# Optimization experiments

Measured on AMD Instinct MI355X. Metric: run time of the kernel, lower is better.

## Reference

```python
import jax, jax.numpy as jnp
import numpy as np
import math

C_S = 256
NUM_HEADS = 8
HEAD_DIM = 32
TOTAL = NUM_HEADS * HEAD_DIM
B, S, I = 1, 256, 256  # batch, msa sequences (column attn axis), residues
LN_EPS = 1e-5


def setup_inputs() -> dict:
    key = jax.random.key(0)
    ks = jax.random.split(key, 10)
    sc = 1.0 / math.sqrt(C_S)
    return {
        "msa": jax.random.normal(ks[0], (B, S, I, C_S), dtype=jnp.float32),
        "ln_gamma": jnp.ones((C_S,), dtype=jnp.float32),
        "ln_beta": jnp.zeros((C_S,), dtype=jnp.float32),
        "Wq": jax.random.normal(ks[1], (C_S, TOTAL), dtype=jnp.float32) * sc,
        "Wk": jax.random.normal(ks[2], (C_S, TOTAL), dtype=jnp.float32) * sc,
        "Wv": jax.random.normal(ks[3], (C_S, TOTAL), dtype=jnp.float32) * sc,
        "Wg": jax.random.normal(ks[4], (C_S, TOTAL), dtype=jnp.float32) * sc,
        "bg": jnp.zeros((TOTAL,), dtype=jnp.float32),
        "Wo": jax.random.normal(ks[5], (TOTAL, C_S), dtype=jnp.float32) * (1.0 / math.sqrt(TOTAL)),
        "bo": jnp.zeros((C_S,), dtype=jnp.float32),
    }


def reference(msa, ln_gamma, ln_beta, Wq, Wk, Wv, Wg, bg, Wo, bo):
    # LayerNorm over channel dim
    mu = jnp.mean(msa, axis=-1, keepdims=True)
    var = jnp.mean(jnp.square(msa - mu), axis=-1, keepdims=True)
    x = (msa - mu) * jax.lax.rsqrt(var + LN_EPS) * ln_gamma + ln_beta

    b, s, i, _ = x.shape
    hd = (NUM_HEADS, HEAD_DIM)
    Q = (x @ Wq).reshape(b, s, i, *hd)
    K = (x @ Wk).reshape(b, s, i, *hd)
    V = (x @ Wv).reshape(b, s, i, *hd)
    G = jax.nn.sigmoid((x @ Wg + bg).reshape(b, s, i, *hd))

    # column attention: contract over head_dim, attend over sequence axis s/t
    scores = jnp.einsum('bsihd,btihd->bihst', Q, K) / math.sqrt(HEAD_DIM)
    attn = jax.nn.softmax(scores, axis=-1)
    vals = jnp.einsum('bihst,btihd->bsihd', attn, V)

    vals = (G * vals).reshape(b, s, i, TOTAL)
    return vals @ Wo + bo
```

## Files before the change

kernel.cpp:

```cpp
#include <hip/hip_runtime.h>
#include <hip/hip_fp16.h>
#include <math.h>

#define C_S 256
#define NUM_HEADS 8
#define HEAD_DIM 32
#define TOTAL 256
#define S_DIM 256
#define I_DIM 256
#define NROWS (S_DIM * I_DIM)
#define LN_EPS 1e-5f
#define QSCALE 0.25503534f

typedef _Float16 f16x8 __attribute__((ext_vector_type(8)));
typedef __attribute__((ext_vector_type(4))) float f32x4;

__device__ __forceinline__ ushort f2h(float x) {
  return __half_as_ushort(__float2half(x));
}
__device__ __forceinline__ float h2f(ushort u) {
  return __half2float(__ushort_as_half(u));
}
__device__ __forceinline__ void gl16(const void* g, void* l) {
  __builtin_amdgcn_global_load_lds(
      (const __attribute__((address_space(1))) unsigned*)g,
      (__attribute__((address_space(3))) unsigned*)l, 16, 0, 0);
}

__global__ __launch_bounds__(256) void prep_w_kernel(
    const float* __restrict__ Wq, const float* __restrict__ Wk,
    const float* __restrict__ Wv, const float* __restrict__ Wg,
    const float* __restrict__ Wo,
    ushort* __restrict__ Wch, ushort* __restrict__ Woh) {
  const int b = blockIdx.x;
  const int mat = b >> 8, n = b & 255;
  const int k = threadIdx.x;
  const float* W = (mat == 0) ? Wq : (mat == 1) ? Wk
                  : (mat == 2) ? Wv : (mat == 3) ? Wg : Wo;
  ushort h = f2h(W[(size_t)k * 256 + n]);
  if (mat < 4) Wch[((size_t)(mat * 256 + n)) * 256 + k] = h;
  else         Woh[(size_t)n * 256 + k] = h;
}

__global__ __launch_bounds__(256) void prep_x_kernel(
    const float* __restrict__ msa, const float* __restrict__ gamma,
    const float* __restrict__ beta, ushort* __restrict__ Xh) {
  const int row  = blockIdx.x * 4 + (threadIdx.x >> 6);
  const int lane = threadIdx.x & 63;
  float4 v = ((const float4*)(msa + (size_t)row * C_S))[lane];
  float sum = v.x + v.y + v.z + v.w;
  float sq  = v.x*v.x + v.y*v.y + v.z*v.z + v.w*v.w;
  #pragma unroll
  for (int off = 1; off < 64; off <<= 1) {
    sum += __shfl_xor(sum, off);
    sq  += __shfl_xor(sq, off);
  }
  float mu = sum * (1.0f / 256.0f);
  float rs = rsqrtf(sq * (1.0f / 256.0f) - mu * mu + LN_EPS);
  float4 gv = ((const float4*)gamma)[lane];
  float4 bv = ((const float4*)beta)[lane];
  ushort4 hh;
  hh.x = f2h((v.x - mu) * rs * gv.x + bv.x);
  hh.y = f2h((v.y - mu) * rs * gv.y + bv.y);
  hh.z = f2h((v.z - mu) * rs * gv.z + bv.z);
  hh.w = f2h((v.w - mu) * rs * gv.w + bv.w);
  *(ushort4*)(Xh + (size_t)row * 256 + lane * 4) = hh;
}

__global__ __launch_bounds__(256, 3) void fused_attn_kernel(
    const ushort* __restrict__ Xh,
    const ushort* __restrict__ Wch,
    const float* __restrict__ bg,
    ushort* __restrict__ Oh) {
  __shared__ __align__(16) ushort Kls[256][40];
  __shared__ __align__(16) ushort Vth[32][264];
  __shared__ __align__(16) ushort Pls[256][32];

  const int bid = blockIdx.x;
  const int xcd = bid & 7, j = bid >> 3;
  const int h = j & 7;
  const int i = (xcd << 5) + (j >> 3);
  const int ih = i * NUM_HEADS + h;
  const int tid = threadIdx.x;
  const int wave = tid >> 6, lane = tid & 63;
  const int lr = lane & 15, quad = lane >> 4;
  const int s_base = wave * 64;
  const size_t hbase = (size_t)ih * (S_DIM * HEAD_DIM);

  const int lrb0 = lr & 1, lrb1 = (lr >> 1) & 1;
  const int qw  = quad ^ (lrb0 << 1);
  const int prd = (quad ^ (lr & 3)) << 3;

  const ushort* xr0 = Xh + ((size_t)(s_base + lr) * 256 + i) * 256 + quad * 8;
  const ushort* wr0 = Wch + ((size_t)(h * 32 + lr)) * 256 + quad * 8;

  f32x4 kacc[2][4] = {}, vacc[2][4] = {};
  #pragma unroll
  for (int kb = 0; kb < 8; ++kb) {
    f16x8 xb[4];
    #pragma unroll
    for (int nt = 0; nt < 4; ++nt)
      xb[nt] = *(const f16x8*)(xr0 + (size_t)nt * 16 * 65536 + kb * 32);
    f16x8 wk[2], wv[2];
    #pragma unroll
    for (int mt = 0; mt < 2; ++mt) {
      wk[mt] = *(const f16x8*)(wr0 + (size_t)1 * 65536 + mt * 4096 + kb * 32);
      wv[mt] = *(const f16x8*)(wr0 + (size_t)2 * 65536 + mt * 4096 + kb * 32);
    }
    #pragma unroll
    for (int mt = 0; mt < 2; ++mt)
      #pragma unroll
      for (int nt = 0; nt < 4; ++nt) {
        kacc[mt][nt] = __builtin_amdgcn_mfma_f32_16x16x32_f16(wk[mt], xb[nt], kacc[mt][nt], 0, 0, 0);
        vacc[mt][nt] = __builtin_amdgcn_mfma_f32_16x16x32_f16(xb[nt], wv[mt], vacc[mt][nt], 0, 0, 0);
      }
  }
  #pragma unroll
  for (int mt = 0; mt < 2; ++mt)
    #pragma unroll
    for (int nt = 0; nt < 4; ++nt) {
      const int t = s_base + nt * 16 + lr;
      ushort4 kp;
      kp.x = f2h(kacc[mt][nt][0]); kp.y = f2h(kacc[mt][nt][1]);
      kp.z = f2h(kacc[mt][nt][2]); kp.w = f2h(kacc[mt][nt][3]);
      *(ushort4*)&Kls[t][mt * 16 + quad * 4] = kp;
      ushort4 vp;
      vp.x = f2h(vacc[mt][nt][0]); vp.y = f2h(vacc[mt][nt][1]);
      vp.z = f2h(vacc[mt][nt][2]); vp.w = f2h(vacc[mt][nt][3]);
      *(ushort4*)&Vth[mt * 16 + lr][s_base + nt * 16 + quad * 4] = vp;
    }

  f32x4 qacc[2][4] = {}, gacc[2][4] = {};
  #pragma unroll
  for (int kb = 0; kb < 8; ++kb) {
    f16x8 xb[4];
    #pragma unroll
    for (int nt = 0; nt < 4; ++nt)
      xb[nt] = *(const f16x8*)(xr0 + (size_t)nt * 16 * 65536 + kb * 32);
    f16x8 wq[2], wg[2];
    #pragma unroll
    for (int mt = 0; mt < 2; ++mt) {
      wq[mt] = *(const f16x8*)(wr0 + (size_t)0 * 65536 + mt * 4096 + kb * 32);
      wg[mt] = *(const f16x8*)(wr0 + (size_t)3 * 65536 + mt * 4096 + kb * 32);
    }
    #pragma unroll
    for (int mt = 0; mt < 2; ++mt)
      #pragma unroll
      for (int nt = 0; nt < 4; ++nt) {
        qacc[mt][nt] = __builtin_amdgcn_mfma_f32_16x16x32_f16(wq[mt], xb[nt], qacc[mt][nt], 0, 0, 0);
        gacc[mt][nt] = __builtin_amdgcn_mfma_f32_16x16x32_f16(wg[mt], xb[nt], gacc[mt][nt], 0, 0, 0);
      }
  }
  #pragma unroll
  for (int mt = 0; mt < 2; ++mt) {
    const int cw = ((mt ^ lrb1) << 4) + (qw << 2);
    #pragma unroll
    for (int nt = 0; nt < 4; ++nt) {
      const int s = s_base + nt * 16 + lr;
      ushort4 qp;
      qp.x = f2h(qacc[mt][nt][0] * QSCALE); qp.y = f2h(qacc[mt][nt][1] * QSCALE);
      qp.z = f2h(qacc[mt][nt][2] * QSCALE); qp.w = f2h(qacc[mt][nt][3] * QSCALE);
      *(ushort4*)&Pls[s][cw] = qp;
    }
  }
  f16x8 qf[4];
  #pragma unroll
  for (int ns = 0; ns < 4; ++ns)
    qf[ns] = *(const f16x8*)&Pls[s_base + ns * 16 + lr][prd];
  f32x4 gv[2][4];
  #pragma unroll
  for (int mt = 0; mt < 2; ++mt) {
    float4 bgv = *(const float4*)(bg + h * 32 + mt * 16 + quad * 4);
    float bga[4] = {bgv.x, bgv.y, bgv.z, bgv.w};
    #pragma unroll
    for (int nt = 0; nt < 4; ++nt)
      #pragma unroll
      for (int reg = 0; reg < 4; ++reg)
        gv[mt][nt][reg] = 1.0f / (1.0f + __expf(-(gacc[mt][nt][reg] + bga[reg])));
  }

  __syncthreads();

  f32x4 oacc[2][4] = {};
  float lpart[4] = {};
  #pragma unroll 1
  for (int c = 0; c < 4; ++c) {
    const int t0 = c * 64;
    f16x8 kf[4];
    #pragma unroll
    for (int mt = 0; mt < 4; ++mt)
      kf[mt] = *(const f16x8*)&Kls[t0 + mt * 16 + lr][quad * 8];
    #pragma unroll
    for (int half = 0; half < 2; ++half) {
      #pragma unroll
      for (int m2 = 0; m2 < 2; ++m2) {
        const int mt = half * 2 + m2;
        const int cw = ((m2 ^ lrb1) << 4) + (qw << 2);
        #pragma unroll
        for (int ns = 0; ns < 4; ++ns) {
          f32x4 sc = {};
          sc = __builtin_amdgcn_mfma_f32_16x16x32_f16(kf[mt], qf[ns], sc, 0, 0, 0);
          float e0 = exp2f(sc[0]), e1 = exp2f(sc[1]);
          float e2 = exp2f(sc[2]), e3 = exp2f(sc[3]);
          lpart[ns] += (e0 + e1) + (e2 + e3);
          ushort4 pk;
          pk.x = f2h(e0); pk.y = f2h(e1); pk.z = f2h(e2); pk.w = f2h(e3);
          *(ushort4*)&Pls[s_base + ns * 16 + lr][cw] = pk;
        }
      }
      const int tq = t0 + half * 32 + quad * 8;
      f16x8 v0 = *(const f16x8*)&Vth[lr][tq];
      f16x8 v1 = *(const f16x8*)&Vth[16 + lr][tq];
      #pragma unroll
      for (int ns = 0; ns < 4; ++ns) {
        f16x8 pf = *(const f16x8*)&Pls[s_base + ns * 16 + lr][prd];
        oacc[0][ns] = __builtin_amdgcn_mfma_f32_16x16x32_f16(v0, pf, oacc[0][ns], 0, 0, 0);
        oacc[1][ns] = __builtin_amdgcn_mfma_f32_16x16x32_f16(v1, pf, oacc[1][ns], 0, 0, 0);
      }
    }
  }

  float invl[4];
  #pragma unroll
  for (int ns = 0; ns < 4; ++ns) {
    float v = lpart[ns];
    v += __shfl_xor(v, 16);
    v += __shfl_xor(v, 32);
    invl[ns] = 1.0f / v;
  }

  #pragma unroll
  for (int ns = 0; ns < 4; ++ns) {
    const int s = s_base + ns * 16 + lr;
    #pragma unroll
    for (int md = 0; md < 2; ++md) {
      const int d0 = md * 16 + quad * 4;
      ushort4 ov;
      ov.x = f2h(gv[md][ns][0] * oacc[md][ns][0] * invl[ns]);
      ov.y = f2h(gv[md][ns][1] * oacc[md][ns][1] * invl[ns]);
      ov.z = f2h(gv[md][ns][2] * oacc[md][ns][2] * invl[ns]);
      ov.w = f2h(gv[md][ns][3] * oacc[md][ns][3] * invl[ns]);
      *(ushort4*)(Oh + hbase + (size_t)s * HEAD_DIM + d0) = ov;
    }
  }
}

__global__ __launch_bounds__(256) void out_kernel(
    const ushort* __restrict__ Oh, const ushort* __restrict__ Woh,
    const float* __restrict__ bo, float* __restrict__ out) {
  __shared__ __align__(16) ushort At0[128 * 32];
  __shared__ __align__(16) ushort At1[128 * 32];
  __shared__ __align__(16) ushort Bt0[128 * 32];
  __shared__ __align__(16) ushort Bt1[128 * 32];

  const int bid = blockIdx.x;
  const int xcd = bid & 7;
  const int j   = bid >> 3;
  const int ntile = j & 1;
  const int rg    = (xcd << 6) + (j >> 1);
  const int n0 = ntile * 128;
  const int s  = rg >> 1;
  const int i0 = (rg & 1) * 128;
  const int tid = threadIdx.x;
  const int wave = tid >> 6, lane = tid & 63;
  const int wm = wave >> 1, wn = wave & 1;
  const int lr = lane & 15, quad = lane >> 4;
  const int fsw = (quad ^ ((lr >> 1) & 3)) * 8;

  const int slot = wave * 64 + lane;
  const int row0 = slot >> 2;
  const int kc   = ((slot & 3) ^ ((row0 >> 1) & 3)) * 8;

  const ushort* pA = Oh + (size_t)(i0 + row0) * 65536 + (size_t)s * 32 + kc;
  const ushort* pB = Woh + (size_t)(n0 + row0) * 256 + kc;
  const int ld0 = wave * 512;
  const int ld1 = 2048 + wave * 512;

  f32x4 acc[4][4] = {};

  for (int kk = 0; kk < 4; ++kk) {
    __syncthreads();
    gl16(pA,               At0 + ld0); gl16(pA + (size_t)64 * 65536,        At0 + ld1);
    gl16(pA + 8192,        At1 + ld0); gl16(pA + (size_t)64 * 65536 + 8192, At1 + ld1);
    gl16(pB,               Bt0 + ld0); gl16(pB + 64 * 256,                  Bt0 + ld1);
    gl16(pB + 32,          Bt1 + ld0); gl16(pB + 64 * 256 + 32,             Bt1 + ld1);
    pA += 16384;
    pB += 64;
    __syncthreads();

    f16x8 a0[4], a1[4], b0[4], b1[4];
    #pragma unroll
    for (int mt = 0; mt < 4; ++mt) {
      const int off = (wm * 64 + mt * 16 + lr) * 32 + fsw;
      a0[mt] = *(const f16x8*)&At0[off];
      a1[mt] = *(const f16x8*)&At1[off];
    }
    #pragma unroll
    for (int nt = 0; nt < 4; ++nt) {
      const int off = (wn * 64 + nt * 16 + lr) * 32 + fsw;
      b0[nt] = *(const f16x8*)&Bt0[off];
      b1[nt] = *(const f16x8*)&Bt1[off];
    }
    #pragma unroll
    for (int mt = 0; mt < 4; ++mt)
      #pragma unroll
      for (int nt = 0; nt < 4; ++nt) {
        acc[mt][nt] = __builtin_amdgcn_mfma_f32_16x16x32_f16(a0[mt], b0[nt], acc[mt][nt], 0, 0, 0);
        acc[mt][nt] = __builtin_amdgcn_mfma_f32_16x16x32_f16(a1[mt], b1[nt], acc[mt][nt], 0, 0, 0);
      }
  }

  #pragma unroll
  for (int nt = 0; nt < 4; ++nt) {
    const int col = n0 + wn * 64 + nt * 16 + lr;
    const float b = bo[col];
    #pragma unroll
    for (int mt = 0; mt < 4; ++mt)
      #pragma unroll
      for (int reg = 0; reg < 4; ++reg) {
        const int mloc = wm * 64 + mt * 16 + quad * 4 + reg;
        out[((size_t)s * 256 + i0 + mloc) * C_S + col] = acc[mt][nt][reg] + b;
      }
  }
}

extern "C" void kernel_launch(void* const* d_in, const int* in_sizes, int n_in,
                              void* d_out, int out_size, void* d_ws, size_t ws_size,
                              hipStream_t stream) {
  const float* msa   = (const float*)d_in[0];
  const float* gamma = (const float*)d_in[1];
  const float* beta  = (const float*)d_in[2];
  const float* Wq    = (const float*)d_in[3];
  const float* Wk    = (const float*)d_in[4];
  const float* Wv    = (const float*)d_in[5];
  const float* Wg    = (const float*)d_in[6];
  const float* bg    = (const float*)d_in[7];
  const float* Wo    = (const float*)d_in[8];
  const float* bo    = (const float*)d_in[9];
  float* out = (float*)d_out;

  const size_t PLANE = (size_t)NROWS * TOTAL;
  ushort* Oh  = (ushort*)d_ws;
  ushort* Wch = Oh + PLANE;
  ushort* Woh = Wch + 1024 * 256;
  ushort* Xh = (ushort*)d_out;

  prep_w_kernel<<<1280, 256, 0, stream>>>(Wq, Wk, Wv, Wg, Wo, Wch, Woh);
  prep_x_kernel<<<NROWS / 4, 256, 0, stream>>>(msa, gamma, beta, Xh);
  fused_attn_kernel<<<I_DIM * NUM_HEADS, 256, 0, stream>>>(Xh, Wch, bg, Oh);
  out_kernel<<<1024, 256, 0, stream>>>(Oh, Woh, bo, out);
}
```

Before: 282.3 us.

## Replace LDS round-trip for Q and P fragments with permlane swaps

Removes the Pls shared-memory buffer and reshapes the Q and softmax-probability MFMA accumulator fragments into B-operand layout in registers, using permlane32/permlane16 swaps. Probabilities are packed with cvt_pkrtz (round-toward-zero) instead of per-element f2h. The sigmoid gate is now computed in the epilogue rather than held live across the attention loop. Occupancy in launch bounds rises from 3 to 4 and setprio is raised around the PV MFMAs. The aim is to cut LDS traffic and LDS footprint, at the cost of possible register pressure and slightly different rounding.

New measurement: 302.8 us. +7.2%, slower.

```diff
diff --git a/kernel.cpp b/kernel.cpp
--- a/kernel.cpp
+++ b/kernel.cpp
@@ -21,10 +21,18 @@
 __device__ __forceinline__ float h2f(ushort u) {
   return __half2float(__ushort_as_half(u));
 }
+__device__ __forceinline__ uint pkrtz(float a, float b) {
+  return __builtin_bit_cast(uint, __builtin_amdgcn_cvt_pkrtz(a, b));
+}
 __device__ __forceinline__ void gl16(const void* g, void* l) {
   __builtin_amdgcn_global_load_lds(
       (const __attribute__((address_space(1))) unsigned*)g,
       (__attribute__((address_space(3))) unsigned*)l, 16, 0, 0);
+}
+__device__ __forceinline__ void quadx(uint x0, uint x1, uint& o0, uint& o1) {
+  auto a = __builtin_amdgcn_permlane32_swap(x0, x1, false, false);
+  auto b = __builtin_amdgcn_permlane16_swap(a[0], a[1], false, false);
+  o0 = b[0]; o1 = b[1];
 }
 
 __global__ __launch_bounds__(256) void prep_w_kernel(
@@ -67,14 +75,13 @@
   *(ushort4*)(Xh + (size_t)row * 256 + lane * 4) = hh;
 }
 
-__global__ __launch_bounds__(256, 3) void fused_attn_kernel(
+__global__ __launch_bounds__(256, 4) void fused_attn_kernel(
     const ushort* __restrict__ Xh,
     const ushort* __restrict__ Wch,
     const float* __restrict__ bg,
     ushort* __restrict__ Oh) {
   __shared__ __align__(16) ushort Kls[256][40];
   __shared__ __align__(16) ushort Vth[32][264];
-  __shared__ __align__(16) ushort Pls[256][32];
 
   const int bid = blockIdx.x;
   const int xcd = bid & 7, j = bid >> 3;
@@ -87,10 +94,6 @@
   const int s_base = wave * 64;
   const size_t hbase = (size_t)ih * (S_DIM * HEAD_DIM);
 
-  const int lrb0 = lr & 1, lrb1 = (lr >> 1) & 1;
-  const int qw  = quad ^ (lrb0 << 1);
-  const int prd = (quad ^ (lr & 3)) << 3;
-
   const ushort* xr0 = Xh + ((size_t)(s_base + lr) * 256 + i) * 256 + quad * 8;
   const ushort* wr0 = Wch + ((size_t)(h * 32 + lr)) * 256 + quad * 8;
 
@@ -151,32 +154,18 @@
         gacc[mt][nt] = __builtin_amdgcn_mfma_f32_16x16x32_f16(wg[mt], xb[nt], gacc[mt][nt], 0, 0, 0);
       }
   }
-  #pragma unroll
-  for (int mt = 0; mt < 2; ++mt) {
-    const int cw = ((mt ^ lrb1) << 4) + (qw << 2);
-    #pragma unroll
-    for (int nt = 0; nt < 4; ++nt) {
-      const int s = s_base + nt * 16 + lr;
-      ushort4 qp;
-      qp.x = f2h(qacc[mt][nt][0] * QSCALE); qp.y = f2h(qacc[mt][nt][1] * QSCALE);
-      qp.z = f2h(qacc[mt][nt][2] * QSCALE); qp.w = f2h(qacc[mt][nt][3] * QSCALE);
-      *(ushort4*)&Pls[s][cw] = qp;
-    }
-  }
   f16x8 qf[4];
   #pragma unroll
-  for (int ns = 0; ns < 4; ++ns)
-    qf[ns] = *(const f16x8*)&Pls[s_base + ns * 16 + lr][prd];
-  f32x4 gv[2][4];
-  #pragma unroll
-  for (int mt = 0; mt < 2; ++mt) {
-    float4 bgv = *(const float4*)(bg + h * 32 + mt * 16 + quad * 4);
-    float bga[4] = {bgv.x, bgv.y, bgv.z, bgv.w};
-    #pragma unroll
-    for (int nt = 0; nt < 4; ++nt)
-      #pragma unroll
-      for (int reg = 0; reg < 4; ++reg)
-        gv[mt][nt][reg] = 1.0f / (1.0f + __expf(-(gacc[mt][nt][reg] + bga[reg])));
+  for (int ns = 0; ns < 4; ++ns) {
+    uint x0 = (uint)f2h(qacc[0][ns][0] * QSCALE) | ((uint)f2h(qacc[0][ns][1] * QSCALE) << 16);
+    uint y0 = (uint)f2h(qacc[0][ns][2] * QSCALE) | ((uint)f2h(qacc[0][ns][3] * QSCALE) << 16);
+    uint x1 = (uint)f2h(qacc[1][ns][0] * QSCALE) | ((uint)f2h(qacc[1][ns][1] * QSCALE) << 16);
+    uint y1 = (uint)f2h(qacc[1][ns][2] * QSCALE) | ((uint)f2h(qacc[1][ns][3] * QSCALE) << 16);
+    uint qa, qb, qc, qd2;
+    quadx(x0, x1, qa, qb);
+    quadx(y0, y1, qc, qd2);
+    uint4 qw4 = make_uint4(qa, qc, qb, qd2);
+    qf[ns] = __builtin_bit_cast(f16x8, qw4);
   }
 
   __syncthreads();
@@ -192,30 +181,30 @@
       kf[mt] = *(const f16x8*)&Kls[t0 + mt * 16 + lr][quad * 8];
     #pragma unroll
     for (int half = 0; half < 2; ++half) {
-      #pragma unroll
-      for (int m2 = 0; m2 < 2; ++m2) {
-        const int mt = half * 2 + m2;
-        const int cw = ((m2 ^ lrb1) << 4) + (qw << 2);
-        #pragma unroll
-        for (int ns = 0; ns < 4; ++ns) {
-          f32x4 sc = {};
-          sc = __builtin_amdgcn_mfma_f32_16x16x32_f16(kf[mt], qf[ns], sc, 0, 0, 0);
-          float e0 = exp2f(sc[0]), e1 = exp2f(sc[1]);
-          float e2 = exp2f(sc[2]), e3 = exp2f(sc[3]);
-          lpart[ns] += (e0 + e1) + (e2 + e3);
-          ushort4 pk;
-          pk.x = f2h(e0); pk.y = f2h(e1); pk.z = f2h(e2); pk.w = f2h(e3);
-          *(ushort4*)&Pls[s_base + ns * 16 + lr][cw] = pk;
-        }
-      }
       const int tq = t0 + half * 32 + quad * 8;
       f16x8 v0 = *(const f16x8*)&Vth[lr][tq];
       f16x8 v1 = *(const f16x8*)&Vth[16 + lr][tq];
       #pragma unroll
       for (int ns = 0; ns < 4; ++ns) {
-        f16x8 pf = *(const f16x8*)&Pls[s_base + ns * 16 + lr][prd];
+        f32x4 s0 = {}, s1 = {};
+        s0 = __builtin_amdgcn_mfma_f32_16x16x32_f16(kf[half * 2 + 0], qf[ns], s0, 0, 0, 0);
+        s1 = __builtin_amdgcn_mfma_f32_16x16x32_f16(kf[half * 2 + 1], qf[ns], s1, 0, 0, 0);
+        float e00 = exp2f(s0[0]), e01 = exp2f(s0[1]);
+        float e02 = exp2f(s0[2]), e03 = exp2f(s0[3]);
+        float e10 = exp2f(s1[0]), e11 = exp2f(s1[1]);
+        float e12 = exp2f(s1[2]), e13 = exp2f(s1[3]);
+        lpart[ns] += ((e00 + e01) + (e02 + e03)) + ((e10 + e11) + (e12 + e13));
+        uint x0 = pkrtz(e00, e01), y0 = pkrtz(e02, e03);
+        uint x1 = pkrtz(e10, e11), y1 = pkrtz(e12, e13);
+        uint pa, pb, pc, pd;
+        quadx(x0, x1, pa, pb);
+        quadx(y0, y1, pc, pd);
+        uint4 pw4 = make_uint4(pa, pc, pb, pd);
+        f16x8 pf = __builtin_bit_cast(f16x8, pw4);
+        __builtin_amdgcn_s_setprio(1);
         oacc[0][ns] = __builtin_amdgcn_mfma_f32_16x16x32_f16(v0, pf, oacc[0][ns], 0, 0, 0);
         oacc[1][ns] = __builtin_amdgcn_mfma_f32_16x16x32_f16(v1, pf, oacc[1][ns], 0, 0, 0);
+        __builtin_amdgcn_s_setprio(0);
       }
     }
   }
@@ -235,11 +224,16 @@
     #pragma unroll
     for (int md = 0; md < 2; ++md) {
       const int d0 = md * 16 + quad * 4;
+      float4 bgv = *(const float4*)(bg + h * 32 + d0);
+      float g0 = 1.0f / (1.0f + __expf(-(gacc[md][ns][0] + bgv.x)));
+      float g1 = 1.0f / (1.0f + __expf(-(gacc[md][ns][1] + bgv.y)));
+      float g2 = 1.0f / (1.0f + __expf(-(gacc[md][ns][2] + bgv.z)));
+      float g3 = 1.0f / (1.0f + __expf(-(gacc[md][ns][3] + bgv.w)));
       ushort4 ov;
-      ov.x = f2h(gv[md][ns][0] * oacc[md][ns][0] * invl[ns]);
-      ov.y = f2h(gv[md][ns][1] * oacc[md][ns][1] * invl[ns]);
-      ov.z = f2h(gv[md][ns][2] * oacc[md][ns][2] * invl[ns]);
-      ov.w = f2h(gv[md][ns][3] * oacc[md][ns][3] * invl[ns]);
+      ov.x = f2h(g0 * oacc[md][ns][0] * invl[ns]);
+      ov.y = f2h(g1 * oacc[md][ns][1] * invl[ns]);
+      ov.z = f2h(g2 * oacc[md][ns][2] * invl[ns]);
+      ov.w = f2h(g3 * oacc[md][ns][3] * invl[ns]);
       *(ushort4*)(Oh + hbase + (size_t)s * HEAD_DIM + d0) = ov;
     }
   }
```
